# Kernel tuning notes

Measured on AMD Instinct MI355X. Metric: run time of the kernel, lower is better.

The kernel has to match this reference:

```python
import jax, jax.numpy as jnp
import numpy as np

EMBED = 1024
HEADS = 16
HEAD_DIM = EMBED // HEADS
NEG = -1e20


def setup_inputs() -> dict:
    key = jax.random.key(0)
    k1, k2, k3, k4, k5, k6 = jax.random.split(key, 6)
    N, S = 2, 2048
    values = jax.random.normal(k1, (N, S, EMBED), dtype=jnp.float32)
    keys = jax.random.normal(k2, (N, S, EMBED), dtype=jnp.float32)
    query = jax.random.normal(k3, (N, S, EMBED), dtype=jnp.float32)
    mask = jax.random.randint(k4, (N, 1, S, S), 0, 2, dtype=jnp.int32)
    # fc_out: Linear(embed, embed) with bias; torch layout W [out, in]
    W_fc = jax.random.normal(k5, (EMBED, EMBED), dtype=jnp.float32) * (1.0 / np.sqrt(EMBED))
    b_fc = jax.random.normal(k6, (EMBED,), dtype=jnp.float32) * 0.01
    return {"values": values, "keys": keys, "query": query, "mask": mask,
            "W_fc": W_fc, "b_fc": b_fc}


def reference(values, keys, query, mask, W_fc, b_fc):
    N, Q, E = query.shape
    K = keys.shape[1]
    H, D = HEADS, HEAD_DIM
    v = values.reshape(N, K, H, D)
    k = keys.reshape(N, K, H, D)
    q = query.reshape(N, Q, H, D)
    # energy: [N, H, Q, K]
    energy = jnp.einsum('nqhd,nkhd->nhqk', q, k)
    energy = jnp.where(mask == 0, NEG, energy)
    # NOTE: original scales by sqrt(embed_size), not sqrt(head_dim)
    attn = jax.nn.softmax(energy / jnp.sqrt(jnp.float32(E)), axis=3)
    out = jnp.einsum('nhqk,nkhd->nqhd', attn, v).reshape(N, Q, H * D)
    return out @ W_fc.T + b_fc
```

## Files before the change

### kernel.cpp

```cpp
#include <hip/hip_runtime.h>
#include <cmath>

#define S_LEN 2048
#define EMB   1024
#define NHEAD 16
#define DHEAD 64
#define PIT   72

typedef __attribute__((ext_vector_type(8)))  short bf16x8;
typedef __attribute__((ext_vector_type(4)))  short bf16x4;
typedef __attribute__((ext_vector_type(4)))  float f32x4;
typedef __attribute__((ext_vector_type(16))) float f32x16;

#define MFMA32(a,b,c) __builtin_amdgcn_mfma_f32_32x32x16_bf16(a,b,c,0,0,0)

__device__ __forceinline__ unsigned short f2bf(float f){
    union { float f; unsigned u; } v; v.f = f;
    unsigned r = v.u + 0x7fffu + ((v.u >> 16) & 1u);
    return (unsigned short)(r >> 16);
}

__device__ __forceinline__ unsigned pk2bf(float a, float b){
#if __has_builtin(__builtin_amdgcn_cvt_pk_bf16_f32)
    typedef __attribute__((ext_vector_type(2))) __bf16 bf2;
    bf2 r = __builtin_amdgcn_cvt_pk_bf16_f32(a, b);
    return *(unsigned*)&r;
#else
    return (unsigned)f2bf(a) | ((unsigned)f2bf(b) << 16);
#endif
}

__device__ __forceinline__ float fast_exp2(float x){
#if __has_builtin(__builtin_amdgcn_exp2f)
    return __builtin_amdgcn_exp2f(x);
#else
    return exp2f(x);
#endif
}

__device__ __forceinline__ float fast_rcp(float x){
#if __has_builtin(__builtin_amdgcn_rcpf)
    return __builtin_amdgcn_rcpf(x);
#else
    return 1.0f / x;
#endif
}

__global__ void prep_all(const float* __restrict__ q, const float* __restrict__ k,
                         const float* __restrict__ v, const int* __restrict__ mask,
                         const float* __restrict__ W,
                         unsigned short* __restrict__ Qb, unsigned short* __restrict__ Kb,
                         unsigned short* __restrict__ Vt, unsigned short* __restrict__ Wb,
                         unsigned* __restrict__ Mb){
    __shared__ unsigned short tile[64*68];
    const int b = blockIdx.x, tid = threadIdx.x;
    if (b < 4096){
        const float SC = 0.045084220027780106f;
        int base = (b*256 + tid) * 4;
        int e = base & (EMB - 1);
        int s = (base >> 10) & (S_LEN - 1);
        int n = base >> 21;
        int h = e >> 6, d = e & 63;
        int dst = ((n*NHEAD + h)*S_LEN + s)*DHEAD + d;
        float4 qv = *(const float4*)(q + base);
        float4 kv = *(const float4*)(k + base);
        uint2 qp, kp;
        qp.x = pk2bf(qv.x*SC, qv.y*SC);
        qp.y = pk2bf(qv.z*SC, qv.w*SC);
        kp.x = pk2bf(kv.x, kv.y);
        kp.y = pk2bf(kv.z, kv.w);
        *(uint2*)(Qb + dst) = qp;
        *(uint2*)(Kb + dst) = kp;
    } else if (b < 5120){
        int idx = b - 4096;
        int st = idx & 31, h = (idx >> 5) & 15, n = idx >> 9;
        int sbase = st * 64;
#pragma unroll
        for (int i = 0; i < 4; i++){
            int c = tid + i*256;
            int srow = c >> 4, c4 = (c & 15) * 4;
            float4 x = *(const float4*)(v + (n*S_LEN + sbase + srow)*EMB + h*DHEAD + c4);
            uint2 p;
            p.x = pk2bf(x.x, x.y);
            p.y = pk2bf(x.z, x.w);
            *(uint2*)&tile[srow*68 + c4] = p;
        }
        __syncthreads();
#pragma unroll
        for (int i = 0; i < 2; i++){
            int c = tid + i*256;
            int d = c >> 3, s8 = (c & 7) * 8;
            unsigned u0 = (unsigned)tile[(s8+0)*68 + d] | ((unsigned)tile[(s8+1)*68 + d] << 16);
            unsigned u1 = (unsigned)tile[(s8+2)*68 + d] | ((unsigned)tile[(s8+3)*68 + d] << 16);
            unsigned u2 = (unsigned)tile[(s8+4)*68 + d] | ((unsigned)tile[(s8+5)*68 + d] << 16);
            unsigned u3 = (unsigned)tile[(s8+6)*68 + d] | ((unsigned)tile[(s8+7)*68 + d] << 16);
            uint4 pk; pk.x = u0; pk.y = u1; pk.z = u2; pk.w = u3;
            *(uint4*)(Vt + ((n*NHEAD + h)*DHEAD + d)*S_LEN + sbase + s8) = pk;
        }
    } else if (b < 6144){
        int base = ((b - 5120)*256 + tid) * 4;
        float4 x = *(const float4*)(W + base);
        uint2 p;
        p.x = pk2bf(x.x, x.y);
        p.y = pk2bf(x.z, x.w);
        *(uint2*)(Wb + base) = p;
    } else {
        int u = (b - 6144)*256 + tid;
        const int4* m4 = (const int4*)mask + (size_t)u*8;
        unsigned w = 0;
#pragma unroll
        for (int i = 0; i < 8; i++){
            int4 m = m4[i];
            unsigned nib = (m.x ? 1u : 0u) | (m.y ? 2u : 0u) | (m.z ? 4u : 0u) | (m.w ? 8u : 0u);
            w |= nib << (i*4);
        }
        Mb[u] = w;
    }
}

__global__ __launch_bounds__(512, 2) void flash_attn(
    const unsigned short* __restrict__ Qb, const unsigned short* __restrict__ Kb,
    const unsigned short* __restrict__ Vt, const unsigned* __restrict__ Mb,
    unsigned short* __restrict__ Ab){
    __shared__ unsigned short Kt[2][64*64];
    __shared__ unsigned short Vl[2][64*64];
    __shared__ uint2 mlut[16];

    const int tid = threadIdx.x;
    if (tid < 16){
        uint2 e;
        e.x = ((tid & 1) ? 0xFFFFu : 0u) | ((tid & 2) ? 0xFFFF0000u : 0u);
        e.y = ((tid & 4) ? 0xFFFFu : 0u) | ((tid & 8) ? 0xFFFF0000u : 0u);
        mlut[tid] = e;
    }

    const int flat = blockIdx.x + (blockIdx.y << 3);
    const int xcd = flat & 7, idx = flat >> 3;
    const int qt = idx & 7;
    const int sl = xcd + ((idx >> 3) << 3);
    const int h = sl & 15, n = sl >> 4;

    const int wave = tid >> 6, lane = tid & 63;
    const int l31 = lane & 31, hi = lane >> 5;
    const int qbase = qt*256 + wave*32;
    const int q = qbase + l31;

    const unsigned short* Qh = Qb + (n*NHEAD + h)*S_LEN*DHEAD;
    const unsigned short* Kh = Kb + (n*NHEAD + h)*S_LEN*DHEAD;
    const unsigned short* Vh = Vt + (n*NHEAD + h)*DHEAD*S_LEN;
    const unsigned* mr = Mb + (size_t)(n*S_LEN + q)*(S_LEN/32);

    const int srow = tid >> 3, schunk = tid & 7;
    const int sdst = srow*64 + ((schunk ^ (srow & 7)) * 8);

    bf16x8 Qf[4];
#pragma unroll
    for (int g = 0; g < 4; g++)
        Qf[g] = *(const bf16x8*)(Qh + q*DHEAD + g*16 + hi*8);

    f32x16 accO0 = (f32x16)0.0f, accO1 = (f32x16)0.0f, accL = (f32x16)0.0f;
    const short onev = 0x3F80;
    const bf16x8 ones8 = {onev,onev,onev,onev,onev,onev,onev,onev};

    uint4 kpre = *(const uint4*)(Kh + srow*DHEAD + schunk*8);
    uint4 vpre = *(const uint4*)(Vh + srow*S_LEN + schunk*8);

    int c = 0;
    for (int kb = 0; kb < S_LEN; kb += 64){
        *(uint4*)&Kt[c][sdst] = kpre;
        *(uint4*)&Vl[c][sdst] = vpre;
        __syncthreads();
        if (kb + 64 < S_LEN){
            kpre = *(const uint4*)(Kh + (kb + 64 + srow)*DHEAD + schunk*8);
            vpre = *(const uint4*)(Vh + srow*S_LEN + kb + 64 + schunk*8);
        }
        uint2 mw = *(const uint2*)(mr + (kb >> 5));

        f32x16 e0 = (f32x16)0.0f, e1 = (f32x16)0.0f;
#pragma unroll
        for (int g = 0; g < 4; g++){
            const int ch = g*2 + hi;
            const int r0 = l31, r1 = 32 + l31;
            bf16x8 kf0 = *(const bf16x8*)&Kt[c][r0*64 + ((ch ^ (r0 & 7))*8)];
            bf16x8 kf1 = *(const bf16x8*)&Kt[c][r1*64 + ((ch ^ (r1 & 7))*8)];
            e0 = MFMA32(kf0, Qf[g], e0);
            e1 = MFMA32(kf1, Qf[g], e1);
        }

        unsigned pw[2][4][2];
#pragma unroll
        for (int t = 0; t < 2; t++){
            const f32x16 ev = t ? e1 : e0;
            unsigned sh = (t ? mw.y : mw.x) >> (4*hi);
#pragma unroll
            for (int s = 0; s < 4; s++){
                uint2 m = mlut[(sh >> (8*s)) & 0xFu];
                float p0 = fast_exp2(ev[4*s+0]);
                float p1 = fast_exp2(ev[4*s+1]);
                float p2 = fast_exp2(ev[4*s+2]);
                float p3 = fast_exp2(ev[4*s+3]);
                pw[t][s][0] = pk2bf(p0, p1) & m.x;
                pw[t][s][1] = pk2bf(p2, p3) & m.y;
            }
        }

#pragma unroll
        for (int t = 0; t < 2; t++){
#pragma unroll
            for (int gg = 0; gg < 2; gg++){
                unsigned a0 = pw[t][2*gg][0],   b0 = pw[t][2*gg+1][0];
                unsigned a1 = pw[t][2*gg][1],   b1 = pw[t][2*gg+1][1];
                asm volatile("v_permlane32_swap_b32 %0, %1" : "+v"(a0), "+v"(b0));
                asm volatile("v_permlane32_swap_b32 %0, %1" : "+v"(a1), "+v"(b1));
                uint4 af; af.x = a0; af.y = a1; af.z = b0; af.w = b1;
                bf16x8 Pa = *(bf16x8*)&af;
                const int kg = t*2 + gg;
                const int ch = kg*2 + hi;
                const int d0 = l31, d1 = 32 + l31;
                bf16x8 vf0 = *(const bf16x8*)&Vl[c][d0*64 + ((ch ^ (d0 & 7))*8)];
                bf16x8 vf1 = *(const bf16x8*)&Vl[c][d1*64 + ((ch ^ (d1 & 7))*8)];
                accO0 = MFMA32(Pa, vf0, accO0);
                accO1 = MFMA32(Pa, vf1, accO1);
                accL  = MFMA32(Pa, ones8, accL);
            }
        }
        c ^= 1;
    }

#pragma unroll
    for (int r = 0; r < 16; r++){
        float inv = fast_rcp(accL[r]);
        int qrow = qbase + (r & 3) + 8*(r >> 2) + 4*hi;
        unsigned short* dst = Ab + (size_t)(n*S_LEN + qrow)*EMB + h*DHEAD + l31;
        dst[0]  = f2bf(accO0[r]*inv);
        dst[32] = f2bf(accO1[r]*inv);
    }
}

__global__ __launch_bounds__(256, 4) void gemm_out(
    const unsigned short* __restrict__ Ab, const unsigned short* __restrict__ W,
    const float* __restrict__ bias, float* __restrict__ out){
    const int flat = blockIdx.x + (blockIdx.y << 4);
    const int xcd = flat & 7, idx = flat >> 3;
    const int nb = idx & 15, mb = xcd*8 + (idx >> 4);
    const int tid = threadIdx.x;
    const int wave = tid >> 6, lane = tid & 63, il = lane & 15, quad = lane >> 4;
    const int wm = wave & 1, wn = wave >> 1;
    const int mbase = mb*64, nbase = nb*64;

    f32x4 acc[2][2];
#pragma unroll
    for (int i = 0; i < 2; i++)
#pragma unroll
        for (int j = 0; j < 2; j++) acc[i][j] = (f32x4){0.f,0.f,0.f,0.f};

    const unsigned short* A0 = Ab + (size_t)(mbase + wm*32 + il)*EMB + quad*8;
    const unsigned short* W0 = W  + (size_t)(nbase + wn*32 + il)*EMB + quad*8;

#pragma unroll
    for (int kb = 0; kb < EMB; kb += 64){
        bf16x8 Af[2][2], Wf[2][2];
#pragma unroll
        for (int mt = 0; mt < 2; mt++)
#pragma unroll
            for (int ks = 0; ks < 2; ks++)
                Af[mt][ks] = *(const bf16x8*)(A0 + (size_t)mt*16*EMB + kb + ks*32);
#pragma unroll
        for (int nt = 0; nt < 2; nt++)
#pragma unroll
            for (int ks = 0; ks < 2; ks++)
                Wf[nt][ks] = *(const bf16x8*)(W0 + (size_t)nt*16*EMB + kb + ks*32);
#pragma unroll
        for (int ks = 0; ks < 2; ks++)
#pragma unroll
            for (int mt = 0; mt < 2; mt++)
#pragma unroll
                for (int nt = 0; nt < 2; nt++)
                    acc[mt][nt] = __builtin_amdgcn_mfma_f32_16x16x32_bf16(Af[mt][ks], Wf[nt][ks], acc[mt][nt], 0, 0, 0);
    }

    float bb[2];
#pragma unroll
    for (int nt = 0; nt < 2; nt++) bb[nt] = bias[nbase + wn*32 + nt*16 + il];
#pragma unroll
    for (int mt = 0; mt < 2; mt++)
#pragma unroll
        for (int r = 0; r < 4; r++){
            int row = mbase + wm*32 + mt*16 + quad*4 + r;
            float* dst = &out[(size_t)row*EMB + nbase + wn*32 + il];
#pragma unroll
            for (int nt = 0; nt < 2; nt++)
                dst[nt*16] = acc[mt][nt][r] + bb[nt];
        }
}

extern "C" void kernel_launch(void* const* d_in, const int* in_sizes, int n_in,
                              void* d_out, int out_size, void* d_ws, size_t ws_size,
                              hipStream_t stream){
    const float* values = (const float*)d_in[0];
    const float* keys   = (const float*)d_in[1];
    const float* query  = (const float*)d_in[2];
    const int*   mask   = (const int*)d_in[3];
    const float* W_fc   = (const float*)d_in[4];
    const float* b_fc   = (const float*)d_in[5];
    float* out = (float*)d_out;

    char* ws = (char*)d_ws;
    unsigned short* Qb  = (unsigned short*)(ws);
    unsigned short* Kb  = (unsigned short*)(ws + (8ull  << 20));
    unsigned short* Vtb = (unsigned short*)(ws + (16ull << 20));
    unsigned short* Wb  = (unsigned short*)(ws + (24ull << 20));
    unsigned*       Mb  = (unsigned*)      (ws + (26ull << 20));
    unsigned short* Ab  = (unsigned short*)(ws + (27ull << 20));

    prep_all  <<<7168, 256, 0, stream>>>(query, keys, values, mask, W_fc,
                                         Qb, Kb, Vtb, Wb, Mb);
    flash_attn<<<dim3(8, 32), 512, 0, stream>>>(Qb, Kb, Vtb, Mb, Ab);
    gemm_out  <<<dim3(16, 64), 256, 0, stream>>>(Ab, Wb, b_fc, out);
}
```

Before: 235.2 us.

## Stage output GEMM tiles in swizzled LDS with register-prefetch double buffering

```diff
diff --git a/kernel.cpp b/kernel.cpp
--- a/kernel.cpp
+++ b/kernel.cpp
@@ -5,7 +5,6 @@
 #define EMB   1024
 #define NHEAD 16
 #define DHEAD 64
-#define PIT   72
 
 typedef __attribute__((ext_vector_type(8)))  short bf16x8;
 typedef __attribute__((ext_vector_type(4)))  short bf16x4;
@@ -237,61 +236,70 @@
     }
 }
 
-__global__ __launch_bounds__(256, 4) void gemm_out(
+__global__ __launch_bounds__(512, 1) void gemm_out(
     const unsigned short* __restrict__ Ab, const unsigned short* __restrict__ W,
     const float* __restrict__ bias, float* __restrict__ out){
-    const int flat = blockIdx.x + (blockIdx.y << 4);
+    __shared__ unsigned short At[2][128*64];
+    __shared__ unsigned short Wt[2][128*64];
+
+    const int flat = blockIdx.x + (blockIdx.y << 3);
     const int xcd = flat & 7, idx = flat >> 3;
-    const int nb = idx & 15, mb = xcd*8 + (idx >> 4);
+    const int nb = idx & 7, mbt = xcd*4 + (idx >> 3);
     const int tid = threadIdx.x;
-    const int wave = tid >> 6, lane = tid & 63, il = lane & 15, quad = lane >> 4;
-    const int wm = wave & 1, wn = wave >> 1;
-    const int mbase = mb*64, nbase = nb*64;
-
-    f32x4 acc[2][2];
-#pragma unroll
-    for (int i = 0; i < 2; i++)
-#pragma unroll
-        for (int j = 0; j < 2; j++) acc[i][j] = (f32x4){0.f,0.f,0.f,0.f};
-
-    const unsigned short* A0 = Ab + (size_t)(mbase + wm*32 + il)*EMB + quad*8;
-    const unsigned short* W0 = W  + (size_t)(nbase + wn*32 + il)*EMB + quad*8;
-
-#pragma unroll
+    const int wave = tid >> 6, lane = tid & 63;
+    const int l31 = lane & 31, hi = lane >> 5;
+    const int wm = wave & 3, wn = wave >> 2;
+    const int mbase = mbt*128, nbase = nb*128;
+    const int am = wm*32, n0 = wn*64;
+
+    const int srow = tid >> 2, sch = tid & 3;
+    const int d0 = srow*64 + ((sch       ^ (srow & 7))*8);
+    const int d1 = srow*64 + (((sch + 4) ^ (srow & 7))*8);
+    const unsigned short* Asrc = Ab + (size_t)(mbase + srow)*EMB + sch*8;
+    const unsigned short* Wsrc = W  + (size_t)(nbase + srow)*EMB + sch*8;
+
+    f32x16 acc0 = (f32x16)0.0f, acc1 = (f32x16)0.0f;
+
+    uint4 apre0 = *(const uint4*)(Asrc);
+    uint4 apre1 = *(const uint4*)(Asrc + 32);
+    uint4 wpre0 = *(const uint4*)(Wsrc);
+    uint4 wpre1 = *(const uint4*)(Wsrc + 32);
+
+    int c = 0;
     for (int kb = 0; kb < EMB; kb += 64){
-        bf16x8 Af[2][2], Wf[2][2];
-#pragma unroll
-        for (int mt = 0; mt < 2; mt++)
-#pragma unroll
-            for (int ks = 0; ks < 2; ks++)
-                Af[mt][ks] = *(const bf16x8*)(A0 + (size_t)mt*16*EMB + kb + ks*32);
-#pragma unroll
-        for (int nt = 0; nt < 2; nt++)
-#pragma unroll
-            for (int ks = 0; ks < 2; ks++)
-                Wf[nt][ks] = *(const bf16x8*)(W0 + (size_t)nt*16*EMB + kb + ks*32);
-#pragma unroll
-        for (int ks = 0; ks < 2; ks++)
-#pragma unroll
-            for (int mt = 0; mt < 2; mt++)
-#pragma unroll
-                for (int nt = 0; nt < 2; nt++)
-                    acc[mt][nt] = __builtin_amdgcn_mfma_f32_16x16x32_bf16(Af[mt][ks], Wf[nt][ks], acc[mt][nt], 0, 0, 0);
-    }
-
-    float bb[2];
-#pragma unroll
-    for (int nt = 0; nt < 2; nt++) bb[nt] = bias[nbase + wn*32 + nt*16 + il];
-#pragma unroll
-    for (int mt = 0; mt < 2; mt++)
-#pragma unroll
-        for (int r = 0; r < 4; r++){
-            int row = mbase + wm*32 + mt*16 + quad*4 + r;
-            float* dst = &out[(size_t)row*EMB + nbase + wn*32 + il];
-#pragma unroll
-            for (int nt = 0; nt < 2; nt++)
-                dst[nt*16] = acc[mt][nt][r] + bb[nt];
-        }
+        *(uint4*)&At[c][d0] = apre0;
+        *(uint4*)&At[c][d1] = apre1;
+        *(uint4*)&Wt[c][d0] = wpre0;
+        *(uint4*)&Wt[c][d1] = wpre1;
+        __syncthreads();
+        if (kb + 64 < EMB){
+            apre0 = *(const uint4*)(Asrc + kb + 64);
+            apre1 = *(const uint4*)(Asrc + kb + 64 + 32);
+            wpre0 = *(const uint4*)(Wsrc + kb + 64);
+            wpre1 = *(const uint4*)(Wsrc + kb + 64 + 32);
+        }
+#pragma unroll
+        for (int kg = 0; kg < 4; kg++){
+            const int ch = kg*2 + hi;
+            const int ra = am + l31, r0 = n0 + l31, r1 = n0 + 32 + l31;
+            bf16x8 Af  = *(const bf16x8*)&At[c][ra*64 + ((ch ^ (ra & 7))*8)];
+            bf16x8 Wf0 = *(const bf16x8*)&Wt[c][r0*64 + ((ch ^ (r0 & 7))*8)];
+            bf16x8 Wf1 = *(const bf16x8*)&Wt[c][r1*64 + ((ch ^ (r1 & 7))*8)];
+            acc0 = MFMA32(Af, Wf0, acc0);
+            acc1 = MFMA32(Af, Wf1, acc1);
+        }
+        c ^= 1;
+    }
+
+    const float b0 = bias[nbase + n0 + l31];
+    const float b1 = bias[nbase + n0 + 32 + l31];
+#pragma unroll
+    for (int r = 0; r < 16; r++){
+        int mrow = mbase + am + (r & 3) + 8*(r >> 2) + 4*hi;
+        float* dst = &out[(size_t)mrow*EMB + nbase + n0 + l31];
+        dst[0]  = acc0[r] + b0;
+        dst[32] = acc1[r] + b1;
+    }
 }
 
 extern "C" void kernel_launch(void* const* d_in, const int* in_sizes, int n_in,
@@ -316,5 +324,5 @@
     prep_all  <<<7168, 256, 0, stream>>>(query, keys, values, mask, W_fc,
                                          Qb, Kb, Vtb, Wb, Mb);
     flash_attn<<<dim3(8, 32), 512, 0, stream>>>(Qb, Kb, Vtb, Mb, Ab);
-    gemm_out  <<<dim3(16, 64), 256, 0, stream>>>(Ab, Wb, b_fc, out);
-}
+    gemm_out  <<<dim3(8, 32), 512, 0, stream>>>(Ab, Wb, b_fc, out);
+}
```

Measured after the change: 196.3 us. 16.5% less time.
